# Performance work log

Measured on AMD Instinct MI355X. Metric: run time of the kernel, lower is better.

The kernel has to match this reference:

```python
import jax, jax.numpy as jnp
from jax import lax
import numpy as np

B, C, H, W = 16, 64, 256, 256
K = 3
PAD = (K - 1) // 2


def setup_inputs() -> dict:
    key = jax.random.key(0)
    ks = jax.random.split(key, 5)
    x = jax.random.normal(ks[0], (B, C, H, W), dtype=jnp.float32)
    # conv1: 1x1 conv dim -> dim*k*k, stored as a (C*K*K, C) matrix since input is (b,c,1,1)
    w1 = jax.random.normal(ks[1], (C * K * K, C), dtype=jnp.float32) * 0.1
    b1 = jax.random.normal(ks[2], (C * K * K,), dtype=jnp.float32) * 0.1
    fscale = jax.random.normal(ks[3], (C,), dtype=jnp.float32) * 0.1
    conv_bias = jax.random.normal(ks[4], (C,), dtype=jnp.float32) * 0.1
    return {"x": x, "w1": w1, "b1": b1, "fscale": fscale, "conv_bias": conv_bias}


def reference(x, w1, b1, fscale, conv_bias):
    b, c, h, w = x.shape
    # global average pool -> (b, c)
    avg = x.mean(axis=(2, 3))
    # 1x1 conv on (b,c,1,1) == dense matmul: (b, c*k*k)
    dyn = avg @ w1.T + b1
    # per-sample, per-channel depthwise kernels, sigmoid-gated
    wk = jax.nn.sigmoid(dyn).reshape(b * c, 1, K, K)  # (b*c, 1, k, k)
    # batch folded into channels -> grouped conv with feature_group_count = b*c
    xf = x.reshape(1, b * c, h, w)
    y = lax.conv_general_dilated(
        xf, wk,
        window_strides=(1, 1),
        padding=[(PAD, PAD), (PAD, PAD)],
        feature_group_count=b * c,
        dimension_numbers=("NCHW", "OIHW", "NCHW"),
    )
    y = y.reshape(b, c, h, w) + conv_bias[None, :, None, None]
    # gated residual blend: (x - y) * fscale * x + y
    fs = fscale[None, :, None, None]
    return (x - y) * fs * x + y
```

## Files before the change

kernel.cpp:

```cpp
#include <hip/hip_runtime.h>
#include <math.h>

#define BB 16
#define CC 64
#define HH 256
#define WW 256
#define HWSZ (HH * WW)
#define NP (BB * CC)
#define STRIPS 4
#define RPW (HH / (STRIPS * 4))

typedef float f4 __attribute__((ext_vector_type(4)));

__global__ __launch_bounds__(256) void mean_kernel(const float* __restrict__ x,
                                                   float* __restrict__ avg) {
    int p = blockIdx.x;
    const float4* xp = (const float4*)(x + (size_t)p * HWSZ);
    float s0 = 0.f, s1 = 0.f, s2 = 0.f, s3 = 0.f;
    for (int i = threadIdx.x; i < HWSZ / 4; i += 1024) {
        float4 a = xp[i];
        float4 b = xp[i + 256];
        float4 c = xp[i + 512];
        float4 d = xp[i + 768];
        s0 += a.x + a.y + a.z + a.w;
        s1 += b.x + b.y + b.z + b.w;
        s2 += c.x + c.y + c.z + c.w;
        s3 += d.x + d.y + d.z + d.w;
    }
    float s = (s0 + s1) + (s2 + s3);
    for (int off = 32; off > 0; off >>= 1) s += __shfl_down(s, off, 64);
    __shared__ float ws[4];
    int lane = threadIdx.x & 63, wid = threadIdx.x >> 6;
    if (lane == 0) ws[wid] = s;
    __syncthreads();
    if (threadIdx.x == 0) {
        avg[p] = (ws[0] + ws[1] + ws[2] + ws[3]) * (1.0f / (float)HWSZ);
    }
}

__global__ __launch_bounds__(256) void wk_kernel(const float* __restrict__ avg,
                                                 const float* __restrict__ w1,
                                                 const float* __restrict__ b1,
                                                 float* __restrict__ wk) {
    int idx = blockIdx.x * 256 + threadIdx.x;
    if (idx >= BB * CC * 9) return;
    int b = idx / (CC * 9);
    int j = idx % (CC * 9);
    const float* a = avg + b * CC;
    const float* wrow = w1 + (size_t)j * CC;
    float s = b1[j];
#pragma unroll
    for (int c2 = 0; c2 < CC; ++c2) s += a[c2] * wrow[c2];
    wk[idx] = 1.0f / (1.0f + expf(-s));
}

__global__ __launch_bounds__(256, 8) void conv_kernel(const float* __restrict__ x,
                                                      const float* __restrict__ wk,
                                                      const float* __restrict__ fscale,
                                                      const float* __restrict__ conv_bias,
                                                      float* __restrict__ out) {
    const int p     = blockIdx.x >> 2;
    const int strip = blockIdx.x & (STRIPS - 1);
    const int wave = threadIdx.x >> 6;
    const int lane = threadIdx.x & 63;
    const int c = p & (CC - 1);
    const int h0 = strip * (HH / STRIPS) + wave * RPW;
    const float* xp = x + (size_t)p * HWSZ;
    float* op = out + (size_t)p * HWSZ;

    const float* wkp = wk + p * 9;
    float k0 = wkp[0], k1 = wkp[1], k2 = wkp[2];
    float k3 = wkp[3], k4 = wkp[4], k5 = wkp[5];
    float k6 = wkp[6], k7 = wkp[7], k8 = wkp[8];
    const float fs = fscale[c];
    const float cb = conv_bias[c];

    auto ldrow = [&](int r) -> f4 {
        if ((unsigned)r < (unsigned)HH) return ((const f4*)(xp + r * WW))[lane];
        return (f4){0.f, 0.f, 0.f, 0.f};
    };
    auto haloL = [&](float w) { float v = __shfl_up(w, 1, 64); return lane == 0 ? 0.f : v; };
    auto haloR = [&](float v0) { float v = __shfl_down(v0, 1, 64); return lane == 63 ? 0.f : v; };

    f4 rp = ldrow(h0 - 1);
    f4 rc = ldrow(h0);
    f4 rn = ldrow(h0 + 1);
    float lp = haloL(rp.w), Rp = haloR(rp.x);
    float lc = haloL(rc.w), Rc = haloR(rc.x);

    for (int h = h0; h < h0 + RPW; ++h) {
        f4 rn2 = ldrow(h + 2);
        float ln = haloL(rn.w), Rn = haloR(rn.x);

        f4 y;
        y.x = cb + k0 * lp   + k1 * rp.x + k2 * rp.y
                 + k3 * lc   + k4 * rc.x + k5 * rc.y
                 + k6 * ln   + k7 * rn.x + k8 * rn.y;
        y.y = cb + k0 * rp.x + k1 * rp.y + k2 * rp.z
                 + k3 * rc.x + k4 * rc.y + k5 * rc.z
                 + k6 * rn.x + k7 * rn.y + k8 * rn.z;
        y.z = cb + k0 * rp.y + k1 * rp.z + k2 * rp.w
                 + k3 * rc.y + k4 * rc.z + k5 * rc.w
                 + k6 * rn.y + k7 * rn.z + k8 * rn.w;
        y.w = cb + k0 * rp.z + k1 * rp.w + k2 * Rp
                 + k3 * rc.z + k4 * rc.w + k5 * Rc
                 + k6 * rn.z + k7 * rn.w + k8 * Rn;

        f4 o;
        o.x = (rc.x - y.x) * fs * rc.x + y.x;
        o.y = (rc.y - y.y) * fs * rc.y + y.y;
        o.z = (rc.z - y.z) * fs * rc.z + y.z;
        o.w = (rc.w - y.w) * fs * rc.w + y.w;
        __builtin_nontemporal_store(o, (f4*)(op + h * WW) + lane);

        rp = rc; rc = rn; rn = rn2;
        lp = lc; Rp = Rc;
        lc = ln; Rc = Rn;
    }
}

extern "C" void kernel_launch(void* const* d_in, const int* in_sizes, int n_in,
                              void* d_out, int out_size, void* d_ws, size_t ws_size,
                              hipStream_t stream) {
    const float* x         = (const float*)d_in[0];
    const float* w1        = (const float*)d_in[1];
    const float* b1        = (const float*)d_in[2];
    const float* fscale    = (const float*)d_in[3];
    const float* conv_bias = (const float*)d_in[4];
    float* out = (float*)d_out;

    float* avg = (float*)d_ws;
    float* wk  = avg + NP;

    mean_kernel<<<NP, 256, 0, stream>>>(x, avg);
    wk_kernel<<<(BB * CC * 9 + 255) / 256, 256, 0, stream>>>(avg, w1, b1, wk);
    conv_kernel<<<NP * STRIPS, 256, 0, stream>>>(x, wk, fscale, conv_bias, out);
}
```

Before: 494.0 us.

## Fuse dynamic kernel computation into conv kernel and process two rows per iteration

```diff
diff --git a/kernel.cpp b/kernel.cpp
--- a/kernel.cpp
+++ b/kernel.cpp
@@ -38,40 +38,36 @@
     }
 }
 
-__global__ __launch_bounds__(256) void wk_kernel(const float* __restrict__ avg,
-                                                 const float* __restrict__ w1,
-                                                 const float* __restrict__ b1,
-                                                 float* __restrict__ wk) {
-    int idx = blockIdx.x * 256 + threadIdx.x;
-    if (idx >= BB * CC * 9) return;
-    int b = idx / (CC * 9);
-    int j = idx % (CC * 9);
-    const float* a = avg + b * CC;
-    const float* wrow = w1 + (size_t)j * CC;
-    float s = b1[j];
-#pragma unroll
-    for (int c2 = 0; c2 < CC; ++c2) s += a[c2] * wrow[c2];
-    wk[idx] = 1.0f / (1.0f + expf(-s));
-}
-
-__global__ __launch_bounds__(256, 8) void conv_kernel(const float* __restrict__ x,
-                                                      const float* __restrict__ wk,
+__global__ __launch_bounds__(256, 4) void conv_kernel(const float* __restrict__ x,
+                                                      const float* __restrict__ avg,
+                                                      const float* __restrict__ w1,
+                                                      const float* __restrict__ b1,
                                                       const float* __restrict__ fscale,
                                                       const float* __restrict__ conv_bias,
                                                       float* __restrict__ out) {
-    const int p     = blockIdx.x >> 2;
-    const int strip = blockIdx.x & (STRIPS - 1);
-    const int wave = threadIdx.x >> 6;
-    const int lane = threadIdx.x & 63;
+    const int p     = blockIdx.x & (NP - 1);
+    const int strip = blockIdx.x >> 10;
+    const int wave  = threadIdx.x >> 6;
+    const int lane  = threadIdx.x & 63;
     const int c = p & (CC - 1);
+    const int b = p >> 6;
     const int h0 = strip * (HH / STRIPS) + wave * RPW;
     const float* xp = x + (size_t)p * HWSZ;
     float* op = out + (size_t)p * HWSZ;
 
-    const float* wkp = wk + p * 9;
-    float k0 = wkp[0], k1 = wkp[1], k2 = wkp[2];
-    float k3 = wkp[3], k4 = wkp[4], k5 = wkp[5];
-    float k6 = wkp[6], k7 = wkp[7], k8 = wkp[8];
+    __shared__ float kk[12];
+    if (threadIdx.x < 9) {
+        const float* a    = avg + b * CC;
+        const float* wrow = w1 + (size_t)(c * 9 + threadIdx.x) * CC;
+        float s = b1[c * 9 + threadIdx.x];
+#pragma unroll
+        for (int c2 = 0; c2 < CC; ++c2) s += a[c2] * wrow[c2];
+        kk[threadIdx.x] = 1.0f / (1.0f + expf(-s));
+    }
+    __syncthreads();
+    const float k0 = kk[0], k1 = kk[1], k2 = kk[2];
+    const float k3 = kk[3], k4 = kk[4], k5 = kk[5];
+    const float k6 = kk[6], k7 = kk[7], k8 = kk[8];
     const float fs = fscale[c];
     const float cb = conv_bias[c];
 
@@ -79,43 +75,69 @@
         if ((unsigned)r < (unsigned)HH) return ((const f4*)(xp + r * WW))[lane];
         return (f4){0.f, 0.f, 0.f, 0.f};
     };
-    auto haloL = [&](float w) { float v = __shfl_up(w, 1, 64); return lane == 0 ? 0.f : v; };
-    auto haloR = [&](float v0) { float v = __shfl_down(v0, 1, 64); return lane == 63 ? 0.f : v; };
+    auto hL = [&](f4 v) { float t = __shfl_up(v.w, 1, 64); return lane == 0 ? 0.f : t; };
+    auto hR = [&](f4 v) { float t = __shfl_down(v.x, 1, 64); return lane == 63 ? 0.f : t; };
 
-    f4 rp = ldrow(h0 - 1);
-    f4 rc = ldrow(h0);
-    f4 rn = ldrow(h0 + 1);
-    float lp = haloL(rp.w), Rp = haloR(rp.x);
-    float lc = haloL(rc.w), Rc = haloR(rc.x);
+    f4 rA = ldrow(h0 - 1);
+    f4 rB = ldrow(h0);
+    f4 rC = ldrow(h0 + 1);
+    f4 rD = ldrow(h0 + 2);
+    float lA = hL(rA), RA = hR(rA);
+    float lB = hL(rB), RB = hR(rB);
+    float lC = hL(rC), RC = hR(rC);
+    float lD = hL(rD), RD = hR(rD);
 
-    for (int h = h0; h < h0 + RPW; ++h) {
-        f4 rn2 = ldrow(h + 2);
-        float ln = haloL(rn.w), Rn = haloR(rn.x);
+    for (int h = h0; h < h0 + RPW; h += 2) {
+        f4 rE = ldrow(h + 3);
+        f4 rF = ldrow(h + 4);
 
-        f4 y;
-        y.x = cb + k0 * lp   + k1 * rp.x + k2 * rp.y
-                 + k3 * lc   + k4 * rc.x + k5 * rc.y
-                 + k6 * ln   + k7 * rn.x + k8 * rn.y;
-        y.y = cb + k0 * rp.x + k1 * rp.y + k2 * rp.z
-                 + k3 * rc.x + k4 * rc.y + k5 * rc.z
-                 + k6 * rn.x + k7 * rn.y + k8 * rn.z;
-        y.z = cb + k0 * rp.y + k1 * rp.z + k2 * rp.w
-                 + k3 * rc.y + k4 * rc.z + k5 * rc.w
-                 + k6 * rn.y + k7 * rn.z + k8 * rn.w;
-        y.w = cb + k0 * rp.z + k1 * rp.w + k2 * Rp
-                 + k3 * rc.z + k4 * rc.w + k5 * Rc
-                 + k6 * rn.z + k7 * rn.w + k8 * Rn;
+        f4 y0;
+        y0.x = cb + k0 * lA   + k1 * rA.x + k2 * rA.y
+                  + k3 * lB   + k4 * rB.x + k5 * rB.y
+                  + k6 * lC   + k7 * rC.x + k8 * rC.y;
+        y0.y = cb + k0 * rA.x + k1 * rA.y + k2 * rA.z
+                  + k3 * rB.x + k4 * rB.y + k5 * rB.z
+                  + k6 * rC.x + k7 * rC.y + k8 * rC.z;
+        y0.z = cb + k0 * rA.y + k1 * rA.z + k2 * rA.w
+                  + k3 * rB.y + k4 * rB.z + k5 * rB.w
+                  + k6 * rC.y + k7 * rC.z + k8 * rC.w;
+        y0.w = cb + k0 * rA.z + k1 * rA.w + k2 * RA
+                  + k3 * rB.z + k4 * rB.w + k5 * RB
+                  + k6 * rC.z + k7 * rC.w + k8 * RC;
+        f4 o0;
+        o0.x = (rB.x - y0.x) * fs * rB.x + y0.x;
+        o0.y = (rB.y - y0.y) * fs * rB.y + y0.y;
+        o0.z = (rB.z - y0.z) * fs * rB.z + y0.z;
+        o0.w = (rB.w - y0.w) * fs * rB.w + y0.w;
+        __builtin_nontemporal_store(o0, (f4*)(op + h * WW) + lane);
 
-        f4 o;
-        o.x = (rc.x - y.x) * fs * rc.x + y.x;
-        o.y = (rc.y - y.y) * fs * rc.y + y.y;
-        o.z = (rc.z - y.z) * fs * rc.z + y.z;
-        o.w = (rc.w - y.w) * fs * rc.w + y.w;
-        __builtin_nontemporal_store(o, (f4*)(op + h * WW) + lane);
+        f4 y1;
+        y1.x = cb + k0 * lB   + k1 * rB.x + k2 * rB.y
+                  + k3 * lC   + k4 * rC.x + k5 * rC.y
+                  + k6 * lD   + k7 * rD.x + k8 * rD.y;
+        y1.y = cb + k0 * rB.x + k1 * rB.y + k2 * rB.z
+                  + k3 * rC.x + k4 * rC.y + k5 * rC.z
+                  + k6 * rD.x + k7 * rD.y + k8 * rD.z;
+        y1.z = cb + k0 * rB.y + k1 * rB.z + k2 * rB.w
+                  + k3 * rC.y + k4 * rC.z + k5 * rC.w
+                  + k6 * rD.y + k7 * rD.z + k8 * rD.w;
+        y1.w = cb + k0 * rB.z + k1 * rB.w + k2 * RB
+                  + k3 * rC.z + k4 * rC.w + k5 * RC
+                  + k6 * rD.z + k7 * rD.w + k8 * RD;
+        f4 o1;
+        o1.x = (rC.x - y1.x) * fs * rC.x + y1.x;
+        o1.y = (rC.y - y1.y) * fs * rC.y + y1.y;
+        o1.z = (rC.z - y1.z) * fs * rC.z + y1.z;
+        o1.w = (rC.w - y1.w) * fs * rC.w + y1.w;
+        __builtin_nontemporal_store(o1, (f4*)(op + (h + 1) * WW) + lane);
 
-        rp = rc; rc = rn; rn = rn2;
-        lp = lc; Rp = Rc;
-        lc = ln; Rc = Rn;
+        float lE = hL(rE), RE = hR(rE);
+        float lF = hL(rF), RF = hR(rF);
+
+        rA = rC; lA = lC; RA = RC;
+        rB = rD; lB = lD; RB = RD;
+        rC = rE; lC = lE; RC = RE;
+        rD = rF; lD = lF; RD = RF;
     }
 }
 
@@ -130,9 +152,7 @@
     float* out = (float*)d_out;
 
     float* avg = (float*)d_ws;
-    float* wk  = avg + NP;
 
     mean_kernel<<<NP, 256, 0, stream>>>(x, avg);
-    wk_kernel<<<(BB * CC * 9 + 255) / 256, 256, 0, stream>>>(avg, w1, b1, wk);
-    conv_kernel<<<NP * STRIPS, 256, 0, stream>>>(x, wk, fscale, conv_bias, out);
+    conv_kernel<<<NP * STRIPS, 256, 0, stream>>>(x, avg, w1, b1, fscale, conv_bias, out);
 }
```

Result: no change. 486.7 us (-1.5%).
